# Performance work log

Hardware: AMD Instinct MI355X
Metric: run time of the kernel (lower is better)

Reference implementation:

```python
import jax, jax.numpy as jnp
import numpy as np

B, N, D = 4, 1024, 1024
H, HD = 16, 64  # num_heads, head_dim


def rotate_half(x):
    x1, x2 = jnp.split(x, 2, axis=-1)
    return jnp.concatenate([-x2, x1], axis=-1)


def setup_inputs() -> dict:
    key = jax.random.key(0)
    ks = jax.random.split(key, 10)
    s = 1.0 / np.sqrt(D)
    hidden_states = jax.random.normal(ks[0], (B, N, D), jnp.float32)
    # rotary angles -> cos/sin per position per head-dim
    ang = jax.random.uniform(ks[1], (B, N, HD), jnp.float32, 0.0, 2 * np.pi)
    cos, sin = jnp.cos(ang), jnp.sin(ang)
    wq = jax.random.normal(ks[2], (D, D), jnp.float32) * s
    bq = jnp.zeros((D,), jnp.float32)
    wk = jax.random.normal(ks[3], (D, D), jnp.float32) * s  # key_bias=False
    wv = jax.random.normal(ks[4], (D, D), jnp.float32) * s
    bv = jnp.zeros((D,), jnp.float32)
    wo = jax.random.normal(ks[5], (D, D), jnp.float32) * s
    bo = jnp.zeros((D,), jnp.float32)
    return {"hidden_states": hidden_states, "cos": cos, "sin": sin,
            "wq": wq, "bq": bq, "wk": wk, "wv": wv, "bv": bv,
            "wo": wo, "bo": bo}


def reference(hidden_states, cos, sin, wq, bq, wk, wv, bv, wo, bo):
    # weights are (out, in) as in eqx Linear: y = x @ W.T + b
    q = jnp.einsum('bnd,ed->bne', hidden_states, wq) + bq
    k = jnp.einsum('bnd,ed->bne', hidden_states, wk)
    v = jnp.einsum('bnd,ed->bne', hidden_states, wv) + bv
    # [B, H, N, HD]
    q = q.reshape(B, N, H, HD).transpose(0, 2, 1, 3)
    k = k.reshape(B, N, H, HD).transpose(0, 2, 1, 3)
    v = v.reshape(B, N, H, HD).transpose(0, 2, 1, 3)
    c = cos[:, None, :, :]  # broadcast over heads
    s = sin[:, None, :, :]
    q = q * c + rotate_half(q) * s
    k = k * c + rotate_half(k) * s
    scale = 1.0 / np.sqrt(HD)
    scores = jnp.einsum('bhqd,bhkd->bhqk', q, k) * scale
    attn = jax.nn.softmax(scores, axis=-1)
    out = jnp.einsum('bhqk,bhkd->bhqd', attn, v)
    out = out.transpose(0, 2, 1, 3).reshape(B, N, D)
    return jnp.einsum('bnd,ed->bne', out, wo) + bo
```

## Files before the change

### kernel.cpp

```cpp
#include <hip/hip_runtime.h>
#include <hip/hip_bf16.h>
#include <cstdint>


typedef _Float16 half8 __attribute__((ext_vector_type(8)));
typedef _Float16 half4 __attribute__((ext_vector_type(4)));
typedef float f32x4 __attribute__((ext_vector_type(4)));

#define DEV_INLINE __device__ __forceinline__

constexpr int Bb = 4, Ns = 1024, Dd = 1024, Hh = 16, HDd = 64;
constexpr int M_ROWS = Bb * Ns;
constexpr int EQKV = 3 * Dd;

constexpr size_t OFF_HSH  = 0;
constexpr size_t SZ_HSH   = (size_t)M_ROWS * Dd * 2;
constexpr size_t OFF_WQKV = OFF_HSH + SZ_HSH;
constexpr size_t SZ_WQKV  = (size_t)EQKV * Dd * 2;
constexpr size_t OFF_WO   = OFF_WQKV + SZ_WQKV;
constexpr size_t SZ_WO    = (size_t)Dd * Dd * 2;
constexpr size_t OFF_BIAS = OFF_WO + SZ_WO;
constexpr size_t OFF_QKV  = OFF_BIAS + 16384;
constexpr size_t SZ_QKV   = (size_t)M_ROWS * EQKV * 2;
constexpr size_t OFF_QT   = OFF_QKV + SZ_QKV;
constexpr size_t SZ_HEADS = (size_t)Bb * Hh * Ns * HDd * 2;
constexpr size_t OFF_KT   = OFF_QT + SZ_HEADS;
constexpr size_t OFF_VT   = OFF_KT + SZ_HEADS;
constexpr size_t OFF_ATTN = OFF_QKV;

DEV_INLINE void async_cp16(const _Float16* g, _Float16* l) {
  __builtin_amdgcn_global_load_lds(
      (const __attribute__((address_space(1))) unsigned int*)(g),
      (__attribute__((address_space(3))) unsigned int*)(l), 16, 0, 0);
}

DEV_INLINE half4 cvt4(float4 v) {
  half4 h;
  h[0] = (_Float16)v.x; h[1] = (_Float16)v.y;
  h[2] = (_Float16)v.z; h[3] = (_Float16)v.w;
  return h;
}

__global__ __launch_bounds__(256) void cvt_kernel(
    const float* __restrict__ hs, const float* __restrict__ wq,
    const float* __restrict__ wk, const float* __restrict__ wv,
    const float* __restrict__ wo, const float* __restrict__ bq,
    const float* __restrict__ bv, _Float16* __restrict__ hsH,
    _Float16* __restrict__ wqkvH, _Float16* __restrict__ woH,
    float* __restrict__ biasP)
{
  const int gid = blockIdx.x * 256 + threadIdx.x;
  const int nHs4 = M_ROWS * Dd / 4;
  const int nW4  = 3 * Dd * Dd / 4;
  const int nWo4 = Dd * Dd / 4;
  if (gid < EQKV / 4) {
#pragma unroll
    for (int j = 0; j < 4; ++j) {
      int e = gid * 4 + j;
      biasP[e] = (e < 1024) ? bq[e] : (e < 2048 ? 0.f : bv[e - 2048]);
    }
  }
  if (gid < nHs4) {
    float4 v = reinterpret_cast<const float4*>(hs)[gid];
    reinterpret_cast<half4*>(hsH)[gid] = cvt4(v);
  } else if (gid < nHs4 + nW4) {
    int j = gid - nHs4;
    const int per = Dd * Dd / 4;
    const float* src = (j < per) ? wq : (j < 2 * per ? wk : wv);
    float4 v = reinterpret_cast<const float4*>(src)[j % per];
    reinterpret_cast<half4*>(wqkvH)[j] = cvt4(v);
  } else if (gid < nHs4 + nW4 + nWo4) {
    int j = gid - nHs4 - nW4;
    float4 v = reinterpret_cast<const float4*>(wo)[j];
    reinterpret_cast<half4*>(woH)[j] = cvt4(v);
  }
}

template<int OUTF32>
__global__ __launch_bounds__(256, 3) void gemm_bt(
    const _Float16* __restrict__ A, const _Float16* __restrict__ Bt,
    const float* __restrict__ bias, void* __restrict__ out,
    int M, int E, int K)
{
  __shared__ _Float16 As[128 * 64];
  __shared__ _Float16 Bs[128 * 64];
  const int t = threadIdx.x;
  const int lane = t & 63, wave = t >> 6;
  const int c15 = lane & 15, g = lane >> 4;
  const int wm = wave >> 1, wn = wave & 1;
  const int m0 = blockIdx.y * 128, e0 = blockIdx.x * 128;

  const int srow  = t >> 3;
  const int scol8 = ((t & 7) ^ ((t >> 3) & 7)) * 8;
  const _Float16* gA0 = A  + (size_t)(m0 + srow) * K + scol8;
  const _Float16* gB0 = Bt + (size_t)(e0 + srow) * K + scol8;
  char* lA = (char*)As + wave * 1024;
  char* lB = (char*)Bs + wave * 1024;

  const char* pA[4][2];
  const char* pB[4][2];
#pragma unroll
  for (int mi = 0; mi < 4; ++mi)
#pragma unroll
    for (int kh = 0; kh < 2; ++kh) {
      int ra = wm * 64 + mi * 16 + c15;
      pA[mi][kh] = (const char*)As + ra * 128 + (((kh * 4 + g) ^ (ra & 7)) << 4);
      int rb = wn * 64 + mi * 16 + c15;
      pB[mi][kh] = (const char*)Bs + rb * 128 + (((kh * 4 + g) ^ (rb & 7)) << 4);
    }

  f32x4 acc[4][4];
  const f32x4 zero = {0.f, 0.f, 0.f, 0.f};
#pragma unroll
  for (int i = 0; i < 4; ++i)
#pragma unroll
    for (int j = 0; j < 4; ++j) acc[i][j] = zero;

  const int nk = K >> 6;
  for (int kt = 0; kt < nk; ++kt) {
    const _Float16* ga = gA0 + kt * 64;
    const _Float16* gb = gB0 + kt * 64;
#pragma unroll
    for (int i = 0; i < 4; ++i) {
      async_cp16(ga + (size_t)(32 * i) * K, (_Float16*)(lA + i * 4096));
      async_cp16(gb + (size_t)(32 * i) * K, (_Float16*)(lB + i * 4096));
    }
    __syncthreads();
#pragma unroll
    for (int kh = 0; kh < 2; ++kh) {
      half8 a[4], b[4];
#pragma unroll
      for (int i = 0; i < 4; ++i) a[i] = *reinterpret_cast<const half8*>(pA[i][kh]);
#pragma unroll
      for (int i = 0; i < 4; ++i) b[i] = *reinterpret_cast<const half8*>(pB[i][kh]);
#pragma unroll
      for (int i = 0; i < 4; ++i)
#pragma unroll
        for (int j = 0; j < 4; ++j)
          acc[i][j] = __builtin_amdgcn_mfma_f32_16x16x32_f16(a[i], b[j], acc[i][j], 0, 0, 0);
    }
    __syncthreads();
  }

#pragma unroll
  for (int i = 0; i < 4; ++i)
#pragma unroll
    for (int j = 0; j < 4; ++j)
#pragma unroll
      for (int r = 0; r < 4; ++r) {
        int row = m0 + wm * 64 + i * 16 + g * 4 + r;
        int col = e0 + wn * 64 + j * 16 + c15;
        float v = acc[i][j][r] + bias[col];
        if (OUTF32)
          reinterpret_cast<float*>(out)[(size_t)row * E + col] = v;
        else
          reinterpret_cast<_Float16*>(out)[(size_t)row * E + col] = (_Float16)v;
      }
}

__global__ __launch_bounds__(256) void rope_kernel(
    const _Float16* __restrict__ qkvH, const float* __restrict__ cosp,
    const float* __restrict__ sinp, _Float16* __restrict__ qTo,
    _Float16* __restrict__ kTo, _Float16* __restrict__ vTo)
{
  __shared__ _Float16 Vs[64 * 72];
  const int t = threadIdx.x;
  const int bx = blockIdx.x;
  const int nt = bx & 15, bh = bx >> 4;
  const int b = bh >> 4, h = bh & 15;
  const int n0 = nt * 64;

#pragma unroll
  for (int sec = 0; sec < 2; ++sec) {
    const int basecol = sec * 1024 + h * 64;
    _Float16* dst = sec ? kTo : qTo;
#pragma unroll
    for (int ii = 0; ii < 8; ++ii) {
      int pid = t + 256 * ii;
      int r = pid >> 5, p = pid & 31;
      int n = n0 + r;
      size_t mrow = (size_t)(b * Ns + n);
      float x1 = (float)qkvH[mrow * EQKV + basecol + p];
      float x2 = (float)qkvH[mrow * EQKV + basecol + 32 + p];
      size_t cso = mrow * HDd;
      float c1 = cosp[cso + p], s1 = sinp[cso + p];
      float c2 = cosp[cso + 32 + p], s2 = sinp[cso + 32 + p];
      _Float16* o = dst + ((size_t)bh * Ns + n) * HDd;
      o[p] = (_Float16)(x1 * c1 - x2 * s1);
      o[32 + p] = (_Float16)(x2 * c2 + x1 * s2);
    }
  }
#pragma unroll
  for (int ii = 0; ii < 2; ++ii) {
    int cid = t + 256 * ii;
    int r = cid >> 3, ch = cid & 7;
    half8 v = *reinterpret_cast<const half8*>(
        qkvH + (size_t)(b * Ns + n0 + r) * EQKV + 2048 + h * 64 + ch * 8);
    *reinterpret_cast<half8*>(&Vs[r * 72 + ch * 8]) = v;
  }
  __syncthreads();
#pragma unroll
  for (int ii = 0; ii < 2; ++ii) {
    int cid = t + 256 * ii;
    int d = cid >> 3, ch = cid & 7;
    half8 w;
#pragma unroll
    for (int kk = 0; kk < 8; ++kk) w[kk] = Vs[(ch * 8 + kk) * 72 + d];
    *reinterpret_cast<half8*>(vTo + ((size_t)bh * HDd + d) * Ns + n0 + ch * 8) = w;
  }
}

__global__ __launch_bounds__(256) void attn_kernel(
    const _Float16* __restrict__ qT, const _Float16* __restrict__ kT,
    const _Float16* __restrict__ vT, _Float16* __restrict__ attnH)
{
  __shared__ _Float16 Ks[64 * 64];
  __shared__ _Float16 Vst[64 * 64];
  __shared__ _Float16 Ps[64 * 64];
  const int t = threadIdx.x;
  const int lane = t & 63, wave = t >> 6;
  const int c = lane & 15, g = lane >> 4;
  const int bx = blockIdx.x;
  const int qt = bx & 15, bh = bx >> 4;
  const int b = bh >> 4, h = bh & 15;
  const int qn0 = qt * 64;
  const int strip = wave * 16;

  const _Float16* qp = qT + ((size_t)bh * Ns + qn0 + strip + c) * HDd + g * 8;
  half8 qf0 = *reinterpret_cast<const half8*>(qp);
  half8 qf1 = *reinterpret_cast<const half8*>(qp + 32);

  half8 ones;
#pragma unroll
  for (int j = 0; j < 8; ++j) ones[j] = (_Float16)1.0f;

  f32x4 accO[4];
  f32x4 accL;
  const f32x4 zero = {0.f, 0.f, 0.f, 0.f};
#pragma unroll
  for (int d = 0; d < 4; ++d) accO[d] = zero;
  accL = zero;

  const half8* pK[2][4];
  const half8* pV[2][4];
  const half8* pP[2];
#pragma unroll
  for (int ks = 0; ks < 2; ++ks) {
#pragma unroll
    for (int i = 0; i < 4; ++i) {
      int rowk = i * 16 + c;
      pK[ks][i] = reinterpret_cast<const half8*>(
          (const char*)Ks + rowk * 128 + ((ks * 64 + g * 16) ^ ((rowk & 7) << 4)));
      int rowv = i * 16 + c;
      pV[ks][i] = reinterpret_cast<const half8*>(
          (const char*)Vst + rowv * 128 + ((ks * 64 + g * 16) ^ ((rowv & 7) << 4)));
    }
    int rowp = strip + c;
    pP[ks] = reinterpret_cast<const half8*>(
        (const char*)Ps + rowp * 128 + ((ks * 64 + g * 16) ^ ((rowp & 7) << 4)));
  }

  const float K1 = 0.18033688011112042f;
  const float K2 = -11.541560327111707f;
  char* prow = (char*)Ps + (strip + c) * 128;
  const int psw = (c & 7) << 4;

  for (int jt = 0; jt < 16; ++jt) {
    __syncthreads();
#pragma unroll
    for (int ii = 0; ii < 2; ++ii) {
      int cid = t + 256 * ii;
      int row = cid >> 3, ch = cid & 7;
      int swz = (ch * 16) ^ ((row & 7) << 4);
      half8 kv = *reinterpret_cast<const half8*>(
          kT + ((size_t)bh * Ns + jt * 64 + row) * HDd + ch * 8);
      *reinterpret_cast<half8*>((char*)Ks + row * 128 + swz) = kv;
      half8 vv = *reinterpret_cast<const half8*>(
          vT + ((size_t)bh * HDd + row) * Ns + jt * 64 + ch * 8);
      *reinterpret_cast<half8*>((char*)Vst + row * 128 + swz) = vv;
    }
    __syncthreads();

    f32x4 s[4];
#pragma unroll
    for (int i = 0; i < 4; ++i) s[i] = zero;
#pragma unroll
    for (int i = 0; i < 4; ++i)
      s[i] = __builtin_amdgcn_mfma_f32_16x16x32_f16(*pK[0][i], qf0, s[i], 0, 0, 0);
#pragma unroll
    for (int i = 0; i < 4; ++i)
      s[i] = __builtin_amdgcn_mfma_f32_16x16x32_f16(*pK[1][i], qf1, s[i], 0, 0, 0);

#pragma unroll
    for (int i = 0; i < 4; ++i) {
      half4 pk;
      pk[0] = (_Float16)__builtin_amdgcn_exp2f(fmaf(s[i][0], K1, K2));
      pk[1] = (_Float16)__builtin_amdgcn_exp2f(fmaf(s[i][1], K1, K2));
      pk[2] = (_Float16)__builtin_amdgcn_exp2f(fmaf(s[i][2], K1, K2));
      pk[3] = (_Float16)__builtin_amdgcn_exp2f(fmaf(s[i][3], K1, K2));
      *reinterpret_cast<half4*>(prow + ((i * 32 + g * 8) ^ psw)) = pk;
    }

#pragma unroll
    for (int ks = 0; ks < 2; ++ks) {
      half8 pa = *pP[ks];
      accL = __builtin_amdgcn_mfma_f32_16x16x32_f16(pa, ones, accL, 0, 0, 0);
#pragma unroll
      for (int dt = 0; dt < 4; ++dt)
        accO[dt] = __builtin_amdgcn_mfma_f32_16x16x32_f16(pa, *pV[ks][dt], accO[dt], 0, 0, 0);
    }
  }

#pragma unroll
  for (int r = 0; r < 4; ++r) {
    float inv = 1.f / accL[r];
    int n = qn0 + strip + g * 4 + r;
#pragma unroll
    for (int dt = 0; dt < 4; ++dt) {
      float v = accO[dt][r] * inv;
      attnH[((size_t)b * Ns + n) * Dd + h * HDd + dt * 16 + c] = (_Float16)v;
    }
  }
}

extern "C" void kernel_launch(void* const* d_in, const int* in_sizes, int n_in,
                              void* d_out, int out_size, void* d_ws, size_t ws_size,
                              hipStream_t stream) {
  const float* hs   = (const float*)d_in[0];
  const float* cosp = (const float*)d_in[1];
  const float* sinp = (const float*)d_in[2];
  const float* wq   = (const float*)d_in[3];
  const float* bq   = (const float*)d_in[4];
  const float* wk   = (const float*)d_in[5];
  const float* wv   = (const float*)d_in[6];
  const float* bv   = (const float*)d_in[7];
  const float* wo   = (const float*)d_in[8];
  const float* bo   = (const float*)d_in[9];

  char* ws = (char*)d_ws;
  _Float16* hsH   = (_Float16*)(ws + OFF_HSH);
  _Float16* wqkvH = (_Float16*)(ws + OFF_WQKV);
  _Float16* woH   = (_Float16*)(ws + OFF_WO);
  float*    biasP = (float*)(ws + OFF_BIAS);
  _Float16* qkvH  = (_Float16*)(ws + OFF_QKV);
  _Float16* qTp   = (_Float16*)(ws + OFF_QT);
  _Float16* kTp   = (_Float16*)(ws + OFF_KT);
  _Float16* vTp   = (_Float16*)(ws + OFF_VT);
  _Float16* attnH = (_Float16*)(ws + OFF_ATTN);

  cvt_kernel<<<8192, 256, 0, stream>>>(hs, wq, wk, wv, wo, bq, bv,
                                       hsH, wqkvH, woH, biasP);
  gemm_bt<0><<<dim3(EQKV / 128, M_ROWS / 128), 256, 0, stream>>>(
      hsH, wqkvH, biasP, qkvH, M_ROWS, EQKV, Dd);
  rope_kernel<<<Bb * Hh * (Ns / 64), 256, 0, stream>>>(qkvH, cosp, sinp,
                                                       qTp, kTp, vTp);
  attn_kernel<<<Bb * Hh * (Ns / 64), 256, 0, stream>>>(qTp, kTp, vTp, attnH);
  gemm_bt<1><<<dim3(Dd / 128, M_ROWS / 128), 256, 0, stream>>>(
      attnH, woH, bo, d_out, M_ROWS, Dd, Dd);
}
```

Before: 112.2 us.

## Double-buffer K/V tiles in attention kernel with register prefetch and MFMA priority

Attention K/V tiles now live in two LDS buffers. The next tile's global loads are issued into registers before the current tile's MFMAs and written to the other buffer afterwards, which removes one of the two barriers per iteration and overlaps global load latency with compute. s_setprio is raised around the MFMA blocks to favour matrix issue. LDS use grows by 16KB per block, which may reduce occupancy, and register pressure rises from holding the prefetched data.

After: 109.2 us. 2.6% less time.

```diff
diff --git a/kernel.cpp b/kernel.cpp
--- a/kernel.cpp
+++ b/kernel.cpp
@@ -214,8 +214,8 @@
     const _Float16* __restrict__ qT, const _Float16* __restrict__ kT,
     const _Float16* __restrict__ vT, _Float16* __restrict__ attnH)
 {
-  __shared__ _Float16 Ks[64 * 64];
-  __shared__ _Float16 Vst[64 * 64];
+  __shared__ _Float16 Ks[2][64 * 64];
+  __shared__ _Float16 Vst[2][64 * 64];
   __shared__ _Float16 Ps[64 * 64];
   const int t = threadIdx.x;
   const int lane = t & 63, wave = t >> 6;
@@ -241,19 +241,23 @@
   for (int d = 0; d < 4; ++d) accO[d] = zero;
   accL = zero;
 
-  const half8* pK[2][4];
-  const half8* pV[2][4];
+  const int srow = t >> 3, sch = t & 7;
+  const int ssw = (sch * 16) ^ ((srow & 7) << 4);
+  const _Float16* gK = kT + ((size_t)bh * Ns + srow) * HDd + sch * 8;
+  const _Float16* gV = vT + ((size_t)bh * HDd + srow) * Ns + sch * 8;
+  char* wKa = (char*)Ks[0]  + srow * 128 + ssw;
+  char* wVa = (char*)Vst[0] + srow * 128 + ssw;
+
+  const char* pK[2][4];
+  const char* pV[2][4];
   const half8* pP[2];
 #pragma unroll
   for (int ks = 0; ks < 2; ++ks) {
 #pragma unroll
     for (int i = 0; i < 4; ++i) {
       int rowk = i * 16 + c;
-      pK[ks][i] = reinterpret_cast<const half8*>(
-          (const char*)Ks + rowk * 128 + ((ks * 64 + g * 16) ^ ((rowk & 7) << 4)));
-      int rowv = i * 16 + c;
-      pV[ks][i] = reinterpret_cast<const half8*>(
-          (const char*)Vst + rowv * 128 + ((ks * 64 + g * 16) ^ ((rowv & 7) << 4)));
+      pK[ks][i] = (const char*)Ks[0]  + rowk * 128 + ((ks * 64 + g * 16) ^ ((rowk & 7) << 4));
+      pV[ks][i] = (const char*)Vst[0] + rowk * 128 + ((ks * 64 + g * 16) ^ ((rowk & 7) << 4));
     }
     int rowp = strip + c;
     pP[ks] = reinterpret_cast<const half8*>(
@@ -265,31 +269,42 @@
   char* prow = (char*)Ps + (strip + c) * 128;
   const int psw = (c & 7) << 4;
 
+  {
+    half8 k0 = *reinterpret_cast<const half8*>(gK);
+    half8 k1 = *reinterpret_cast<const half8*>(gK + 32 * HDd);
+    half8 v0 = *reinterpret_cast<const half8*>(gV);
+    half8 v1 = *reinterpret_cast<const half8*>(gV + 32 * Ns);
+    *reinterpret_cast<half8*>(wKa) = k0;
+    *reinterpret_cast<half8*>(wKa + 4096) = k1;
+    *reinterpret_cast<half8*>(wVa) = v0;
+    *reinterpret_cast<half8*>(wVa + 4096) = v1;
+  }
+  __syncthreads();
+
   for (int jt = 0; jt < 16; ++jt) {
-    __syncthreads();
-#pragma unroll
-    for (int ii = 0; ii < 2; ++ii) {
-      int cid = t + 256 * ii;
-      int row = cid >> 3, ch = cid & 7;
-      int swz = (ch * 16) ^ ((row & 7) << 4);
-      half8 kv = *reinterpret_cast<const half8*>(
-          kT + ((size_t)bh * Ns + jt * 64 + row) * HDd + ch * 8);
-      *reinterpret_cast<half8*>((char*)Ks + row * 128 + swz) = kv;
-      half8 vv = *reinterpret_cast<const half8*>(
-          vT + ((size_t)bh * HDd + row) * Ns + jt * 64 + ch * 8);
-      *reinterpret_cast<half8*>((char*)Vst + row * 128 + swz) = vv;
-    }
-    __syncthreads();
+    const int bo = (jt & 1) * 8192;
+    const bool pre = (jt + 1 < 16);
+    half8 kr0, kr1, vr0, vr1;
+    if (pre) {
+      kr0 = *reinterpret_cast<const half8*>(gK + (jt + 1) * 4096);
+      kr1 = *reinterpret_cast<const half8*>(gK + (jt + 1) * 4096 + 32 * HDd);
+      vr0 = *reinterpret_cast<const half8*>(gV + (jt + 1) * 64);
+      vr1 = *reinterpret_cast<const half8*>(gV + (jt + 1) * 64 + 32 * Ns);
+    }
 
     f32x4 s[4];
 #pragma unroll
     for (int i = 0; i < 4; ++i) s[i] = zero;
+    __builtin_amdgcn_s_setprio(1);
 #pragma unroll
     for (int i = 0; i < 4; ++i)
-      s[i] = __builtin_amdgcn_mfma_f32_16x16x32_f16(*pK[0][i], qf0, s[i], 0, 0, 0);
+      s[i] = __builtin_amdgcn_mfma_f32_16x16x32_f16(
+          *reinterpret_cast<const half8*>(pK[0][i] + bo), qf0, s[i], 0, 0, 0);
 #pragma unroll
     for (int i = 0; i < 4; ++i)
-      s[i] = __builtin_amdgcn_mfma_f32_16x16x32_f16(*pK[1][i], qf1, s[i], 0, 0, 0);
+      s[i] = __builtin_amdgcn_mfma_f32_16x16x32_f16(
+          *reinterpret_cast<const half8*>(pK[1][i] + bo), qf1, s[i], 0, 0, 0);
+    __builtin_amdgcn_s_setprio(0);
 
 #pragma unroll
     for (int i = 0; i < 4; ++i) {
@@ -301,13 +316,25 @@
       *reinterpret_cast<half4*>(prow + ((i * 32 + g * 8) ^ psw)) = pk;
     }
 
+    __builtin_amdgcn_s_setprio(1);
 #pragma unroll
     for (int ks = 0; ks < 2; ++ks) {
       half8 pa = *pP[ks];
       accL = __builtin_amdgcn_mfma_f32_16x16x32_f16(pa, ones, accL, 0, 0, 0);
 #pragma unroll
       for (int dt = 0; dt < 4; ++dt)
-        accO[dt] = __builtin_amdgcn_mfma_f32_16x16x32_f16(pa, *pV[ks][dt], accO[dt], 0, 0, 0);
+        accO[dt] = __builtin_amdgcn_mfma_f32_16x16x32_f16(
+            pa, *reinterpret_cast<const half8*>(pV[ks][dt] + bo), accO[dt], 0, 0, 0);
+    }
+    __builtin_amdgcn_s_setprio(0);
+
+    if (pre) {
+      const int wo_ = 8192 - bo;
+      *reinterpret_cast<half8*>(wKa + wo_) = kr0;
+      *reinterpret_cast<half8*>(wKa + wo_ + 4096) = kr1;
+      *reinterpret_cast<half8*>(wVa + wo_) = vr0;
+      *reinterpret_cast<half8*>(wVa + wo_ + 4096) = vr1;
+      __syncthreads();
     }
   }
 
```
